# Performance work log

Hardware: AMD Instinct MI355X
Metric: run time of the kernel (lower is better)

## Reference

```python
import jax, jax.numpy as jnp
import numpy as np

B, S, D, H = 2, 2048, 1024, 16
HD = D // H  # head dim = 64

def setup_inputs() -> dict:
    key = jax.random.key(0)
    ks = jax.random.split(key, 3)
    scale = 1.0 / np.sqrt(D)
    return {
        "x": jax.random.normal(ks[0], (B, S, D), jnp.float32),
        "W_attn": jax.random.normal(ks[1], (D, 3 * D), jnp.float32) * scale,
        "b_attn": jnp.zeros((3 * D,), jnp.float32),
        "W_proj": jax.random.normal(ks[2], (D, D), jnp.float32) * scale,
        "b_proj": jnp.zeros((D,), jnp.float32),
    }

def reference(x, W_attn, b_attn, W_proj, b_proj):
    b, s, d = x.shape
    qkv = x @ W_attn + b_attn                      # [B,S,3D]
    q, k, v = jnp.split(qkv, 3, axis=-1)
    # [B,S,D] -> [B,H,S,HD]
    def heads(t):
        return t.reshape(b, s, H, HD).transpose(0, 2, 1, 3)
    q, k, v = heads(q), heads(k), heads(v)
    scores = jnp.einsum('bhqd,bhkd->bhqk', q, k) * (1.0 / np.sqrt(HD))
    causal = jnp.tril(jnp.ones((s, s), dtype=bool))
    scores = jnp.where(causal[None, None], scores, -jnp.inf)
    probs = jax.nn.softmax(scores, axis=-1)
    y = jnp.einsum('bhqk,bhkd->bhqd', probs, v)    # [B,H,S,HD]
    y = y.transpose(0, 2, 1, 3).reshape(b, s, d)
    return y @ W_proj + b_proj
```

## Files before the change

### kernel.cpp

```cpp
#include <hip/hip_runtime.h>

typedef __bf16 bf16;
typedef __bf16 bf16x4 __attribute__((ext_vector_type(4)));
typedef __bf16 bf16x8 __attribute__((ext_vector_type(8)));
typedef float f32x4 __attribute__((ext_vector_type(4)));

#define S_LEN 2048
#define D_DIM 1024
#define N_HEAD 16
#define HEAD_DIM 64
#define M_TOK 4096
#define BH 32

#define EXP2F(x) __builtin_amdgcn_exp2f(x)
#define Q_SCALE 0.18033688f
#define RESCALE_THR 8.0f

#define SW8(r, c) ((c) ^ (((r) & 7) << 3))
#define SWG(r, c) ((c) ^ ((((r) >> 1) & 3) << 3))
#define SIG(r) (((r) & 0x23) | (((r) & 0x04) << 2) | (((r) & 0x18) >> 1))
#define SIGINV(y) (((y) & 0x23) | (((y) >> 2) & 0x04) | (((y) & 0x0C) << 1))

typedef __attribute__((address_space(3))) void lds_void;
typedef const __attribute__((address_space(1))) void gbl_void;

__device__ __forceinline__ void gl_lds16(const bf16* g, bf16* l) {
  __builtin_amdgcn_global_load_lds((gbl_void*)g, (lds_void*)l, 16, 0, 0);
}

__global__ __launch_bounds__(256) void k_cast(const float* __restrict__ x,
                                              bf16* __restrict__ o, int n) {
  int i = (blockIdx.x * 256 + threadIdx.x) * 4;
  if (i >= n) return;
  float4 v = *(const float4*)(x + i);
  bf16x4 w;
  w[0] = (bf16)v.x; w[1] = (bf16)v.y; w[2] = (bf16)v.z; w[3] = (bf16)v.w;
  *(bf16x4*)(o + i) = w;
}

__global__ __launch_bounds__(256) void k_transpose(const float* __restrict__ W,
                                                   bf16* __restrict__ Wt,
                                                   int K, int N) {
  __shared__ float tile[32][33];
  int nb = blockIdx.x, kb = blockIdx.y;
  int t = threadIdx.x;
  int r = t >> 3, c4 = (t & 7) * 4;
  float4 v = *(const float4*)&W[(kb * 32 + r) * N + nb * 32 + c4];
  tile[r][c4 + 0] = v.x; tile[r][c4 + 1] = v.y;
  tile[r][c4 + 2] = v.z; tile[r][c4 + 3] = v.w;
  __syncthreads();
  bf16x4 o;
  #pragma unroll
  for (int i = 0; i < 4; i++) o[i] = (bf16)tile[c4 + i][r];
  *(bf16x4*)&Wt[(nb * 32 + r) * K + kb * 32 + c4] = o;
}

__global__ __launch_bounds__(256, 4)
void k_gemm_qkv(const bf16* __restrict__ A, const bf16* __restrict__ Bt,
                const float* __restrict__ bias,
                bf16* __restrict__ qk, bf16* __restrict__ vT) {
  __shared__ bf16 As[2][128 * 32];
  __shared__ bf16 Bs[2][128 * 32];
  const int K = 1024;
  int bn = blockIdx.x, bm = blockIdx.y;
  int t = threadIdx.x;
  int wave = t >> 6, lane = t & 63, c = lane & 15, quad = lane >> 4;
  int wm = wave & 1, wn = wave >> 1;
  int ldrow = lane >> 2;
  int ldcol = (((lane & 3) ^ ((lane >> 3) & 3)) * 8);

  const bf16* Ag = A + (size_t)(bm * 128) * K;
  const bf16* Bg = Bt + (size_t)(bn * 128) * K;

  f32x4 acc[4][4] = {};

  #pragma unroll
  for (int q = 0; q < 2; q++) {
    int r0 = (wave * 2 + q) * 16;
    gl_lds16(&Ag[(size_t)(r0 + ldrow) * K + ldcol], &As[0][r0 * 32]);
    gl_lds16(&Bg[(size_t)(r0 + ldrow) * K + ldcol], &Bs[0][r0 * 32]);
  }

  int cur = 0;
  for (int k0 = 0; k0 < K; k0 += 32, cur ^= 1) {
    __syncthreads();
    if (k0 + 32 < K) {
      int nxt = cur ^ 1;
      #pragma unroll
      for (int q = 0; q < 2; q++) {
        int r0 = (wave * 2 + q) * 16;
        gl_lds16(&Ag[(size_t)(r0 + ldrow) * K + k0 + 32 + ldcol], &As[nxt][r0 * 32]);
        gl_lds16(&Bg[(size_t)(r0 + ldrow) * K + k0 + 32 + ldcol], &Bs[nxt][r0 * 32]);
      }
    }
    bf16x8 af[4];
    #pragma unroll
    for (int mt = 0; mt < 4; mt++) {
      int ar = wm * 64 + mt * 16 + c;
      af[mt] = *(const bf16x8*)&As[cur][ar * 32 + SWG(ar, quad * 8)];
    }
    #pragma unroll
    for (int nt = 0; nt < 4; nt++) {
      int br = wn * 64 + nt * 16 + c;
      bf16x8 bfr = *(const bf16x8*)&Bs[cur][br * 32 + SWG(br, quad * 8)];
      #pragma unroll
      for (int mt = 0; mt < 4; mt++)
        acc[mt][nt] = __builtin_amdgcn_mfma_f32_16x16x32_bf16(af[mt], bfr, acc[mt][nt], 0, 0, 0);
    }
  }

  #pragma unroll
  for (int nt = 0; nt < 4; nt++) {
    int n = bn * 128 + wn * 64 + nt * 16 + c;
    int which = n >> 10, nl = n & 1023;
    int h = nl >> 6, hd = nl & 63;
    float bv = bias[n];
    #pragma unroll
    for (int mt = 0; mt < 4; mt++) {
      int m0 = bm * 128 + wm * 64 + mt * 16 + quad * 4;
      int b = m0 >> 11, s0 = m0 & 2047;
      int bh = b * N_HEAD + h;
      if (which == 2) {
        bf16x4 o;
        #pragma unroll
        for (int r = 0; r < 4; r++) o[r] = (bf16)(acc[mt][nt][r] + bv);
        *(bf16x4*)&vT[((size_t)bh * HEAD_DIM + hd) * S_LEN + s0] = o;
      } else if (which == 0) {
        #pragma unroll
        for (int r = 0; r < 4; r++)
          qk[(bh * S_LEN + s0 + r) * HEAD_DIM + hd] = (bf16)((acc[mt][nt][r] + bv) * Q_SCALE);
      } else {
        #pragma unroll
        for (int r = 0; r < 4; r++)
          qk[BH * S_LEN * HEAD_DIM + (bh * S_LEN + s0 + r) * HEAD_DIM + hd] = (bf16)(acc[mt][nt][r] + bv);
      }
    }
  }
}

__global__ __launch_bounds__(256, 2)
void k_attn(const bf16* __restrict__ qk, const bf16* __restrict__ vT,
            bf16* __restrict__ y) {
  __shared__ bf16 Ks[2][128][64];
  __shared__ bf16 Vs[2][64][128];
  int bx = blockIdx.x;
  int bh, p;
  if (bx < 256) { bh = bx & 31; p = bx >> 5; }
  else          { int j = bx - 256; bh = j & 31; p = 15 - (j >> 5); }
  int t = threadIdx.x, w = t >> 6, lane = t & 63, c = lane & 15, quad = lane >> 4;
  const bf16* Qg = qk + (size_t)bh * (S_LEN * HEAD_DIM);
  const bf16* Kg = qk + (size_t)(BH + bh) * (S_LEN * HEAD_DIM);
  const bf16* Vg = vT + (size_t)bh * (HEAD_DIM * S_LEN);
  int b = bh >> 4, h = bh & 15;

  const int NKB2 = p + 1;
  const int dthrA = w * 32 + c;
  const int dthrB = dthrA + 16;

  int baseK = w * 8 + (lane >> 3);
  int cK  = (((lane & 7) ^ (baseK & 7)) << 3);
  const bf16* kSrc = Kg + (size_t)SIGINV(baseK) * HEAD_DIM + cK;
  int baseV = w * 4 + (lane >> 4);
  int cV  = (((lane & 15) ^ (baseV & 7)) << 3);
  const bf16* vSrc = Vg + (size_t)baseV * S_LEN + cV;

  #pragma unroll
  for (int i = 0; i < 4; i++) {
    gl_lds16(kSrc + (size_t)(32 * i) * HEAD_DIM, &Ks[0][w * 8 + 32 * i][0]);
    gl_lds16(vSrc + (size_t)(16 * i) * S_LEN,    &Vs[0][w * 4 + 16 * i][0]);
  }

  bf16x8 qfA[2], qfB[2];
  f32x4 accA[4] = {}, accB[4] = {};
  float mMA = -1e30f, lLA = 0.f, mMB = -1e30f, lLB = 0.f;
  {
    int qrA = p * 128 + w * 32 + c;
    qfA[0] = *(const bf16x8*)&Qg[qrA * HEAD_DIM + quad * 8];
    qfA[1] = *(const bf16x8*)&Qg[qrA * HEAD_DIM + 32 + quad * 8];
    int qrB = qrA + 16;
    qfB[0] = *(const bf16x8*)&Qg[qrB * HEAD_DIM + quad * 8];
    qfB[1] = *(const bf16x8*)&Qg[qrB * HEAD_DIM + 32 + quad * 8];
  }

  for (int kb2 = 0; kb2 < NKB2; kb2++) {
    __syncthreads();
    int cur = kb2 & 1, nxt = cur ^ 1;
    if (kb2 + 1 < NKB2) {
      size_t ko = (size_t)(kb2 + 1) * (128 * HEAD_DIM);
      int    vo = (kb2 + 1) * 128;
      #pragma unroll
      for (int i = 0; i < 4; i++) {
        gl_lds16(kSrc + ko + (size_t)(32 * i) * HEAD_DIM, &Ks[nxt][w * 8 + 32 * i][0]);
        gl_lds16(vSrc + vo + (size_t)(16 * i) * S_LEN,    &Vs[nxt][w * 4 + 16 * i][0]);
      }
    }

    f32x4 scA[8], scB[8];
    __builtin_amdgcn_s_setprio(1);
    #pragma unroll
    for (int kt = 0; kt < 8; kt++) {
      int krr = kt * 16 + c;
      bf16x8 kf0 = *(const bf16x8*)&Ks[cur][krr][SW8(krr, quad * 8)];
      bf16x8 kf1 = *(const bf16x8*)&Ks[cur][krr][SW8(krr, 32 + quad * 8)];
      f32x4 za = {};
      za = __builtin_amdgcn_mfma_f32_16x16x32_bf16(kf0, qfA[0], za, 0, 0, 0);
      za = __builtin_amdgcn_mfma_f32_16x16x32_bf16(kf1, qfA[1], za, 0, 0, 0);
      scA[kt] = za;
      f32x4 zb = {};
      zb = __builtin_amdgcn_mfma_f32_16x16x32_bf16(kf0, qfB[0], zb, 0, 0, 0);
      zb = __builtin_amdgcn_mfma_f32_16x16x32_bf16(kf1, qfB[1], zb, 0, 0, 0);
      scB[kt] = zb;
    }
    __builtin_amdgcn_s_setprio(0);

    if (kb2 == p) {
      #pragma unroll
      for (int kt = 0; kt < 8; kt++) {
        int kbase = ((kt >> 2) << 6) + (((kt >> 1) & 1) << 5) + quad * 8 + ((kt & 1) << 2);
        #pragma unroll
        for (int r = 0; r < 4; r++) {
          if (kbase + r > dthrA) scA[kt][r] = -1e30f;
          if (kbase + r > dthrB) scB[kt][r] = -1e30f;
        }
      }
    }

    bf16x8 pfA[4], pfB[4];
    {
      float tmA[8], tmB[8];
      #pragma unroll
      for (int kt = 0; kt < 8; kt++) {
        tmA[kt] = fmaxf(fmaxf(scA[kt][0], scA[kt][1]), fmaxf(scA[kt][2], scA[kt][3]));
        tmB[kt] = fmaxf(fmaxf(scB[kt][0], scB[kt][1]), fmaxf(scB[kt][2], scB[kt][3]));
      }
      float mxA = fmaxf(fmaxf(fmaxf(tmA[0], tmA[1]), fmaxf(tmA[2], tmA[3])),
                        fmaxf(fmaxf(tmA[4], tmA[5]), fmaxf(tmA[6], tmA[7])));
      float mxB = fmaxf(fmaxf(fmaxf(tmB[0], tmB[1]), fmaxf(tmB[2], tmB[3])),
                        fmaxf(fmaxf(tmB[4], tmB[5]), fmaxf(tmB[6], tmB[7])));
      mxA = fmaxf(mxA, __shfl_xor(mxA, 16));
      mxB = fmaxf(mxB, __shfl_xor(mxB, 16));
      mxA = fmaxf(mxA, __shfl_xor(mxA, 32));
      mxB = fmaxf(mxB, __shfl_xor(mxB, 32));
      bool small = (mxA <= mMA + RESCALE_THR) && (mxB <= mMB + RESCALE_THR);
      if (!__all(small)) {
        float mnA = fmaxf(mMA, mxA), mnB = fmaxf(mMB, mxB);
        float alA = EXP2F(mMA - mnA), alB = EXP2F(mMB - mnB);
        mMA = mnA; mMB = mnB;
        lLA *= alA; lLB *= alB;
        #pragma unroll
        for (int dt = 0; dt < 4; dt++)
          #pragma unroll
          for (int r = 0; r < 4; r++) { accA[dt][r] *= alA; accB[dt][r] *= alB; }
      }
      float ssA[4] = {0.f, 0.f, 0.f, 0.f}, ssB[4] = {0.f, 0.f, 0.f, 0.f};
      #pragma unroll
      for (int kt = 0; kt < 8; kt++) {
        #pragma unroll
        for (int r = 0; r < 4; r++) {
          float ea = EXP2F(scA[kt][r] - mMA);
          float eb = EXP2F(scB[kt][r] - mMB);
          pfA[kt >> 1][(kt & 1) * 4 + r] = (bf16)ea;
          pfB[kt >> 1][(kt & 1) * 4 + r] = (bf16)eb;
          ssA[r] += ea; ssB[r] += eb;
        }
      }
      float sA = (ssA[0] + ssA[1]) + (ssA[2] + ssA[3]);
      float sB = (ssB[0] + ssB[1]) + (ssB[2] + ssB[3]);
      sA += __shfl_xor(sA, 16);
      sB += __shfl_xor(sB, 16);
      sA += __shfl_xor(sA, 32);
      sB += __shfl_xor(sB, 32);
      lLA += sA; lLB += sB;
    }

    __builtin_amdgcn_s_setprio(1);
    #pragma unroll
    for (int ks = 0; ks < 4; ks++) {
      #pragma unroll
      for (int dt = 0; dt < 4; dt++) {
        int vrow = dt * 16 + c;
        bf16x8 vf = *(const bf16x8*)&Vs[cur][vrow][SW8(vrow, ks * 32 + quad * 8)];
        accA[dt] = __builtin_amdgcn_mfma_f32_16x16x32_bf16(vf, pfA[ks], accA[dt], 0, 0, 0);
        accB[dt] = __builtin_amdgcn_mfma_f32_16x16x32_bf16(vf, pfB[ks], accB[dt], 0, 0, 0);
      }
    }
    __builtin_amdgcn_s_setprio(0);
  }

  {
    int qA = p * 128 + w * 32 + c;
    int qB = qA + 16;
    float liA = 1.0f / lLA, liB = 1.0f / lLB;
    #pragma unroll
    for (int dt = 0; dt < 4; dt++) {
      bf16x4 oA, oB;
      #pragma unroll
      for (int r = 0; r < 4; r++) {
        oA[r] = (bf16)(accA[dt][r] * liA);
        oB[r] = (bf16)(accB[dt][r] * liB);
      }
      *(bf16x4*)&y[((size_t)(b * S_LEN + qA) * N_HEAD + h) * HEAD_DIM + dt * 16 + quad * 4] = oA;
      *(bf16x4*)&y[((size_t)(b * S_LEN + qB) * N_HEAD + h) * HEAD_DIM + dt * 16 + quad * 4] = oB;
    }
  }
}

__global__ __launch_bounds__(256, 4)
void k_gemm_proj(const bf16* __restrict__ A, const bf16* __restrict__ Bt,
                 const float* __restrict__ bias, float* __restrict__ out) {
  __shared__ bf16 As[2][128 * 32];
  __shared__ bf16 Bs[2][64 * 32];
  const int K = 1024;
  int bn = blockIdx.x, bm = blockIdx.y;
  int t = threadIdx.x;
  int wave = t >> 6, lane = t & 63, c = lane & 15, quad = lane >> 4;
  int wm = wave & 1, wn = wave >> 1;
  int ldrow = lane >> 2;
  int ldcol = (((lane & 3) ^ ((lane >> 3) & 3)) * 8);

  const bf16* Ag = A + (size_t)(bm * 128) * K;
  const bf16* Bg = Bt + (size_t)(bn * 64) * K;

  f32x4 acc[4][2] = {};

  #pragma unroll
  for (int q = 0; q < 2; q++) {
    int r0 = (wave * 2 + q) * 16;
    gl_lds16(&Ag[(size_t)(r0 + ldrow) * K + ldcol], &As[0][r0 * 32]);
  }
  gl_lds16(&Bg[(size_t)(wave * 16 + ldrow) * K + ldcol], &Bs[0][wave * 16 * 32]);

  int cur = 0;
  for (int k0 = 0; k0 < K; k0 += 32, cur ^= 1) {
    __syncthreads();
    if (k0 + 32 < K) {
      int nxt = cur ^ 1;
      #pragma unroll
      for (int q = 0; q < 2; q++) {
        int r0 = (wave * 2 + q) * 16;
        gl_lds16(&Ag[(size_t)(r0 + ldrow) * K + k0 + 32 + ldcol], &As[nxt][r0 * 32]);
      }
      gl_lds16(&Bg[(size_t)(wave * 16 + ldrow) * K + k0 + 32 + ldcol], &Bs[nxt][wave * 16 * 32]);
    }
    bf16x8 af[4];
    #pragma unroll
    for (int mt = 0; mt < 4; mt++) {
      int ar = wm * 64 + mt * 16 + c;
      af[mt] = *(const bf16x8*)&As[cur][ar * 32 + SWG(ar, quad * 8)];
    }
    #pragma unroll
    for (int nt = 0; nt < 2; nt++) {
      int br = wn * 32 + nt * 16 + c;
      bf16x8 bfr = *(const bf16x8*)&Bs[cur][br * 32 + SWG(br, quad * 8)];
      #pragma unroll
      for (int mt = 0; mt < 4; mt++)
        acc[mt][nt] = __builtin_amdgcn_mfma_f32_16x16x32_bf16(af[mt], bfr, acc[mt][nt], 0, 0, 0);
    }
  }

  #pragma unroll
  for (int nt = 0; nt < 2; nt++) {
    int n = bn * 64 + wn * 32 + nt * 16 + c;
    float bv = bias[n];
    #pragma unroll
    for (int mt = 0; mt < 4; mt++) {
      #pragma unroll
      for (int r = 0; r < 4; r++) {
        int m = bm * 128 + wm * 64 + mt * 16 + quad * 4 + r;
        out[(size_t)m * D_DIM + n] = acc[mt][nt][r] + bv;
      }
    }
  }
}

extern "C" void kernel_launch(void* const* d_in, const int* in_sizes, int n_in,
                              void* d_out, int out_size, void* d_ws, size_t ws_size,
                              hipStream_t stream) {
  const float* x      = (const float*)d_in[0];
  const float* W_attn = (const float*)d_in[1];
  const float* b_attn = (const float*)d_in[2];
  const float* W_proj = (const float*)d_in[3];
  const float* b_proj = (const float*)d_in[4];
  float* out = (float*)d_out;

  bf16* x_bf = (bf16*)d_ws;
  bf16* wat  = x_bf + 4096 * 1024;
  bf16* wpt  = wat + 3072 * 1024;
  bf16* qk   = wpt + 1024 * 1024;
  bf16* vT   = qk + 8 * 1024 * 1024;
  bf16* y_bf = vT + 4 * 1024 * 1024;

  k_cast<<<4096, 256, 0, stream>>>(x, x_bf, 4096 * 1024);
  k_transpose<<<dim3(3072 / 32, 1024 / 32), 256, 0, stream>>>(W_attn, wat, 1024, 3072);
  k_transpose<<<dim3(1024 / 32, 1024 / 32), 256, 0, stream>>>(W_proj, wpt, 1024, 1024);
  k_gemm_qkv<<<dim3(24, 32), 256, 0, stream>>>(x_bf, wat, b_attn, qk, vT);
  k_attn<<<512, 256, 0, stream>>>(qk, vT, y_bf);
  k_gemm_proj<<<dim3(16, 32), 256, 0, stream>>>(y_bf, wpt, b_proj, out);
}
```

Measured before the change: 183.3 us.

## Split long causal attention rows into KV chunks with a separate merge kernel

Each q-tile of 8 or more in the causal attention kernel now has its KV range split into two chunks, handled by separate blocks. A constant table schedules 24 chunks per head, ordered longest first, and the grid grows from 512 to 768 blocks. Split chunks write unnormalized fp32 accumulators plus their max and sum to workspace, and a new merge kernel combines the two halves with log-sum-exp rescaling. The aim is to balance per-block work and fill the GPU better; the cost is an extra launch, extra fp32 partial traffic, and more workspace.

```diff
diff --git a/kernel.cpp b/kernel.cpp
--- a/kernel.cpp
+++ b/kernel.cpp
@@ -20,6 +20,10 @@
 #define SWG(r, c) ((c) ^ ((((r) >> 1) & 3) << 3))
 #define SIG(r) (((r) & 0x23) | (((r) & 0x04) << 2) | (((r) & 0x18) >> 1))
 #define SIGINV(y) (((y) & 0x23) | (((y) >> 2) & 0x04) | (((y) & 0x0C) << 1))
+
+__device__ __constant__ int CH_TILE[24] = {15,15,14, 7,14,13,13,12, 6,12,11,11,10, 5,10, 9, 9, 8, 4, 8, 3, 2, 1, 0};
+__device__ __constant__ int CH_ST  [24] = { 0, 8, 0, 0, 8, 0, 7, 0, 0, 7, 0, 6, 0, 0, 6, 0, 5, 0, 0, 5, 0, 0, 0, 0};
+__device__ __constant__ int CH_LEN [24] = { 8, 8, 8, 8, 7, 7, 7, 7, 7, 6, 6, 6, 6, 6, 5, 5, 5, 5, 5, 4, 4, 3, 2, 1};
 
 typedef __attribute__((address_space(3))) void lds_void;
 typedef const __attribute__((address_space(1))) void gbl_void;
@@ -140,20 +144,23 @@
 
 __global__ __launch_bounds__(256, 2)
 void k_attn(const bf16* __restrict__ qk, const bf16* __restrict__ vT,
-            bf16* __restrict__ y) {
+            bf16* __restrict__ y, float* __restrict__ pacc,
+            float* __restrict__ pml) {
   __shared__ bf16 Ks[2][128][64];
   __shared__ bf16 Vs[2][64][128];
   int bx = blockIdx.x;
-  int bh, p;
-  if (bx < 256) { bh = bx & 31; p = bx >> 5; }
-  else          { int j = bx - 256; bh = j & 31; p = 15 - (j >> 5); }
+  int cid = bx >> 5, bh = bx & 31;
+  int p   = CH_TILE[cid];
+  int kbS = CH_ST[cid];
+  int kbL = CH_LEN[cid];
+  bool split   = (p >= 8);
+  bool hasDiag = (kbS + kbL == p + 1);
   int t = threadIdx.x, w = t >> 6, lane = t & 63, c = lane & 15, quad = lane >> 4;
   const bf16* Qg = qk + (size_t)bh * (S_LEN * HEAD_DIM);
   const bf16* Kg = qk + (size_t)(BH + bh) * (S_LEN * HEAD_DIM);
   const bf16* Vg = vT + (size_t)bh * (HEAD_DIM * S_LEN);
   int b = bh >> 4, h = bh & 15;
 
-  const int NKB2 = p + 1;
   const int dthrA = w * 32 + c;
   const int dthrB = dthrA + 16;
 
@@ -164,10 +171,14 @@
   int cV  = (((lane & 15) ^ (baseV & 7)) << 3);
   const bf16* vSrc = Vg + (size_t)baseV * S_LEN + cV;
 
-  #pragma unroll
-  for (int i = 0; i < 4; i++) {
-    gl_lds16(kSrc + (size_t)(32 * i) * HEAD_DIM, &Ks[0][w * 8 + 32 * i][0]);
-    gl_lds16(vSrc + (size_t)(16 * i) * S_LEN,    &Vs[0][w * 4 + 16 * i][0]);
+  {
+    size_t ko = (size_t)kbS * (128 * HEAD_DIM);
+    int    vo = kbS * 128;
+    #pragma unroll
+    for (int i = 0; i < 4; i++) {
+      gl_lds16(kSrc + ko + (size_t)(32 * i) * HEAD_DIM, &Ks[0][w * 8 + 32 * i][0]);
+      gl_lds16(vSrc + vo + (size_t)(16 * i) * S_LEN,    &Vs[0][w * 4 + 16 * i][0]);
+    }
   }
 
   bf16x8 qfA[2], qfB[2];
@@ -182,16 +193,16 @@
     qfB[1] = *(const bf16x8*)&Qg[qrB * HEAD_DIM + 32 + quad * 8];
   }
 
-  for (int kb2 = 0; kb2 < NKB2; kb2++) {
+  for (int i = 0; i < kbL; i++) {
     __syncthreads();
-    int cur = kb2 & 1, nxt = cur ^ 1;
-    if (kb2 + 1 < NKB2) {
-      size_t ko = (size_t)(kb2 + 1) * (128 * HEAD_DIM);
-      int    vo = (kb2 + 1) * 128;
-      #pragma unroll
-      for (int i = 0; i < 4; i++) {
-        gl_lds16(kSrc + ko + (size_t)(32 * i) * HEAD_DIM, &Ks[nxt][w * 8 + 32 * i][0]);
-        gl_lds16(vSrc + vo + (size_t)(16 * i) * S_LEN,    &Vs[nxt][w * 4 + 16 * i][0]);
+    int cur = i & 1, nxt = cur ^ 1;
+    if (i + 1 < kbL) {
+      size_t ko = (size_t)(kbS + i + 1) * (128 * HEAD_DIM);
+      int    vo = (kbS + i + 1) * 128;
+      #pragma unroll
+      for (int j = 0; j < 4; j++) {
+        gl_lds16(kSrc + ko + (size_t)(32 * j) * HEAD_DIM, &Ks[nxt][w * 8 + 32 * j][0]);
+        gl_lds16(vSrc + vo + (size_t)(16 * j) * S_LEN,    &Vs[nxt][w * 4 + 16 * j][0]);
       }
     }
 
@@ -213,7 +224,7 @@
     }
     __builtin_amdgcn_s_setprio(0);
 
-    if (kb2 == p) {
+    if (hasDiag && i == kbL - 1) {
       #pragma unroll
       for (int kt = 0; kt < 8; kt++) {
         int kbase = ((kt >> 2) << 6) + (((kt >> 1) & 1) << 5) + quad * 8 + ((kt & 1) << 2);
@@ -287,8 +298,10 @@
     __builtin_amdgcn_s_setprio(0);
   }
 
-  {
-    int qA = p * 128 + w * 32 + c;
+  int rowA = w * 32 + c;
+  int rowB = rowA + 16;
+  if (!split) {
+    int qA = p * 128 + rowA;
     int qB = qA + 16;
     float liA = 1.0f / lLA, liB = 1.0f / lLB;
     #pragma unroll
@@ -302,6 +315,54 @@
       *(bf16x4*)&y[((size_t)(b * S_LEN + qA) * N_HEAD + h) * HEAD_DIM + dt * 16 + quad * 4] = oA;
       *(bf16x4*)&y[((size_t)(b * S_LEN + qB) * N_HEAD + h) * HEAD_DIM + dt * 16 + quad * 4] = oB;
     }
+  } else {
+    int ci = kbS ? 1 : 0;
+    size_t base = ((size_t)((p - 8) * 32 + bh) * 2 + ci);
+    float* pa = pacc + base * (128 * 64);
+    float* pm = pml + base * 256;
+    #pragma unroll
+    for (int dt = 0; dt < 4; dt++) {
+      *(float4*)&pa[rowA * 64 + dt * 16 + quad * 4] = *(float4*)&accA[dt];
+      *(float4*)&pa[rowB * 64 + dt * 16 + quad * 4] = *(float4*)&accB[dt];
+    }
+    if (quad == 0) {
+      pm[rowA] = mMA; pm[128 + rowA] = lLA;
+      pm[rowB] = mMB; pm[128 + rowB] = lLB;
+    }
+  }
+}
+
+__global__ __launch_bounds__(256)
+void k_merge(const float* __restrict__ pacc, const float* __restrict__ pml,
+             bf16* __restrict__ y) {
+  int g = blockIdx.x;
+  int pt = g >> 5, bh = g & 31;
+  int p = pt + 8;
+  int b = bh >> 4, h = bh & 15;
+  int t = threadIdx.x;
+  int row = t >> 1, half = (t & 1) * 32;
+  size_t base0 = (size_t)g * 2 * (128 * 64);
+  size_t base1 = base0 + 128 * 64;
+  size_t ml0 = (size_t)g * 2 * 256;
+  size_t ml1 = ml0 + 256;
+  float m0 = pml[ml0 + row], l0 = pml[ml0 + 128 + row];
+  float m1 = pml[ml1 + row], l1 = pml[ml1 + 128 + row];
+  float m = fmaxf(m0, m1);
+  float a0 = EXP2F(m0 - m), a1 = EXP2F(m1 - m);
+  float linv = 1.0f / (a0 * l0 + a1 * l1);
+  a0 *= linv; a1 *= linv;
+  int q = p * 128 + row;
+  bf16* yo = y + ((size_t)(b * S_LEN + q) * N_HEAD + h) * HEAD_DIM + half;
+  #pragma unroll
+  for (int cc = 0; cc < 32; cc += 4) {
+    float4 v0 = *(const float4*)&pacc[base0 + row * 64 + half + cc];
+    float4 v1 = *(const float4*)&pacc[base1 + row * 64 + half + cc];
+    bf16x4 o;
+    o[0] = (bf16)(a0 * v0.x + a1 * v1.x);
+    o[1] = (bf16)(a0 * v0.y + a1 * v1.y);
+    o[2] = (bf16)(a0 * v0.z + a1 * v1.z);
+    o[3] = (bf16)(a0 * v0.w + a1 * v1.w);
+    *(bf16x4*)&yo[cc] = o;
   }
 }
 
@@ -389,11 +450,14 @@
   bf16* qk   = wpt + 1024 * 1024;
   bf16* vT   = qk + 8 * 1024 * 1024;
   bf16* y_bf = vT + 4 * 1024 * 1024;
+  float* pacc = (float*)(y_bf + 4 * 1024 * 1024);
+  float* pml  = pacc + (size_t)8 * 32 * 2 * 128 * 64;
 
   k_cast<<<4096, 256, 0, stream>>>(x, x_bf, 4096 * 1024);
   k_transpose<<<dim3(3072 / 32, 1024 / 32), 256, 0, stream>>>(W_attn, wat, 1024, 3072);
   k_transpose<<<dim3(1024 / 32, 1024 / 32), 256, 0, stream>>>(W_proj, wpt, 1024, 1024);
   k_gemm_qkv<<<dim3(24, 32), 256, 0, stream>>>(x_bf, wat, b_attn, qk, vT);
-  k_attn<<<512, 256, 0, stream>>>(qk, vT, y_bf);
+  k_attn<<<768, 256, 0, stream>>>(qk, vT, y_bf, pacc, pml);
+  k_merge<<<256, 256, 0, stream>>>(pacc, pml, y_bf);
   k_gemm_proj<<<dim3(16, 32), 256, 0, stream>>>(y_bf, wpt, b_proj, out);
 }
```

New measurement: 188.5 us. +2.9%, slower.
